# Kernel optimization log

Hardware: AMD Instinct MI355X
Metric: run time of the kernel (lower is better)

Reference implementation:

```python
import jax, jax.numpy as jnp
import numpy as np

CROP_H = 216
CROP_W = 216
NUM_CROPS = 8


def setup_inputs() -> dict:
    key = jax.random.key(0)
    k1, k2, k3 = jax.random.split(key, 3)
    B, C, H, W = 64, 3, 240, 240
    images = jax.random.normal(k1, (B, C, H, W), dtype=jnp.float32)
    crop_inds_h = jax.random.randint(k2, (B, NUM_CROPS), 0, H - CROP_H, dtype=jnp.int32)
    crop_inds_w = jax.random.randint(k3, (B, NUM_CROPS), 0, W - CROP_W, dtype=jnp.int32)
    return {"images": images, "crop_inds_h": crop_inds_h, "crop_inds_w": crop_inds_w}


def reference(images, crop_inds_h, crop_inds_w):
    # CropRandomizer.forward_in with pos_enc=True.
    B, C, H, W = images.shape
    # positional encoding channels: normalized (y, x) source-pixel coordinates
    yy, xx = jnp.meshgrid(
        jnp.arange(H, dtype=jnp.float32) / H,
        jnp.arange(W, dtype=jnp.float32) / W,
        indexing="ij",
    )
    pos = jnp.stack((yy, xx))                       # [2, H, W]
    pos = jnp.broadcast_to(pos[None], (B, 2, H, W)) # [B, 2, H, W]
    src = jnp.concatenate((images, pos), axis=1)    # [B, C+2, H, W]
    Cp = C + 2

    def crop_one(img, h0, w0):
        # img: [Cp, H, W]; h0, w0 scalar ints
        return jax.lax.dynamic_slice(img, (0, h0, w0), (Cp, CROP_H, CROP_W))

    per_image = jax.vmap(lambda img, hs, ws: jax.vmap(lambda h, w: crop_one(img, h, w))(hs, ws))
    crops = per_image(src, crop_inds_h, crop_inds_w)  # [B, N, Cp, CROP_H, CROP_W]
    return crops.reshape(B * NUM_CROPS, Cp, CROP_H, CROP_W)
```

## Files before the change

kernel.cpp:

```cpp
#include <hip/hip_runtime.h>


#define CROP_HW   216
#define N_CROPS   8
#define IMG_B     64
#define IMG_C     3
#define IMG_H     240
#define IMG_W     240
#define CP        5

#define ROW4      (CROP_HW / 4)
#define PLANE4    (CROP_HW * ROW4)
#define CROP4     (CP * PLANE4)

__global__ __launch_bounds__(256) void crop_pos_kernel(
    const float* __restrict__ images,
    const int*   __restrict__ ch,
    const int*   __restrict__ cw,
    float4*      __restrict__ out,
    unsigned int total4)
{
    const float inv = 1.0f / 240.0f;
    unsigned int stride = gridDim.x * blockDim.x;
    for (unsigned int idx = blockIdx.x * blockDim.x + threadIdx.x;
         idx < total4; idx += stride) {

        unsigned int n    = idx / CROP4;
        unsigned int rem  = idx - n * CROP4;
        unsigned int c    = rem / PLANE4;
        unsigned int rem2 = rem - c * PLANE4;
        unsigned int i    = rem2 / ROW4;
        unsigned int j    = (rem2 - i * ROW4) * 4;

        unsigned int b  = n >> 3;
        unsigned int cr = n & 7;
        int h0 = ch[b * N_CROPS + cr];
        int w0 = cw[b * N_CROPS + cr];

        float4 v;
        if (c < IMG_C) {
            const float* src = images
                + (((b * IMG_C + c) * IMG_H) + (unsigned)(h0 + (int)i)) * IMG_W
                + (unsigned)(w0 + (int)j);
            v.x = src[0]; v.y = src[1]; v.z = src[2]; v.w = src[3];
        } else if (c == 3) {
            float val = (float)(h0 + (int)i) * inv;
            v.x = val; v.y = val; v.z = val; v.w = val;
        } else {
            float base = (float)(w0 + (int)j) * inv;
            v.x = base;
            v.y = base + inv;
            v.z = base + 2.0f * inv;
            v.w = base + 3.0f * inv;
        }
        out[idx] = v;
    }
}

extern "C" void kernel_launch(void* const* d_in, const int* in_sizes, int n_in,
                              void* d_out, int out_size, void* d_ws, size_t ws_size,
                              hipStream_t stream) {
    const float* images = (const float*)d_in[0];
    const int*   ch     = (const int*)d_in[1];
    const int*   cw     = (const int*)d_in[2];
    float4*      out    = (float4*)d_out;

    unsigned int total4 = (unsigned int)(out_size / 4);
    dim3 block(256);
    dim3 grid(2048);
    crop_pos_kernel<<<grid, block, 0, stream>>>(images, ch, cw, out, total4);
}
```

Measured before the change: 533.7 us.

## Assign one block per crop plane with nontemporal vector stores

Replaces the grid-stride loop over flattened output indices with one block per (crop, channel) plane. Crop offsets and the channel branch become block-uniform, and per-element index division is reduced. Output writes use nontemporal stores so the large write stream bypasses cache retention. The fixed grid is now tied to 512 crops, so the launch no longer depends on the output size.

```diff
diff --git a/kernel.cpp b/kernel.cpp
--- a/kernel.cpp
+++ b/kernel.cpp
@@ -3,7 +3,6 @@
 
 #define CROP_HW   216
 #define N_CROPS   8
-#define IMG_B     64
 #define IMG_C     3
 #define IMG_H     240
 #define IMG_W     240
@@ -13,47 +12,58 @@
 #define PLANE4    (CROP_HW * ROW4)
 #define CROP4     (CP * PLANE4)
 
+typedef float f32x4 __attribute__((ext_vector_type(4)));
+
 __global__ __launch_bounds__(256) void crop_pos_kernel(
     const float* __restrict__ images,
     const int*   __restrict__ ch,
     const int*   __restrict__ cw,
-    float4*      __restrict__ out,
-    unsigned int total4)
+    f32x4*       __restrict__ out)
 {
     const float inv = 1.0f / 240.0f;
-    unsigned int stride = gridDim.x * blockDim.x;
-    for (unsigned int idx = blockIdx.x * blockDim.x + threadIdx.x;
-         idx < total4; idx += stride) {
 
-        unsigned int n    = idx / CROP4;
-        unsigned int rem  = idx - n * CROP4;
-        unsigned int c    = rem / PLANE4;
-        unsigned int rem2 = rem - c * PLANE4;
-        unsigned int i    = rem2 / ROW4;
-        unsigned int j    = (rem2 - i * ROW4) * 4;
+    unsigned int blk = blockIdx.x;
+    unsigned int n   = blk / CP;
+    unsigned int c   = blk - n * CP;
+    unsigned int b   = n >> 3;
+    unsigned int cr  = n & 7;
 
-        unsigned int b  = n >> 3;
-        unsigned int cr = n & 7;
-        int h0 = ch[b * N_CROPS + cr];
-        int w0 = cw[b * N_CROPS + cr];
+    int h0 = ch[b * N_CROPS + cr];
+    int w0 = cw[b * N_CROPS + cr];
 
-        float4 v;
-        if (c < IMG_C) {
-            const float* src = images
-                + (((b * IMG_C + c) * IMG_H) + (unsigned)(h0 + (int)i)) * IMG_W
-                + (unsigned)(w0 + (int)j);
-            v.x = src[0]; v.y = src[1]; v.z = src[2]; v.w = src[3];
-        } else if (c == 3) {
+    f32x4* outp = out + (size_t)n * CROP4 + (size_t)c * PLANE4;
+
+    if (c < IMG_C) {
+        const float* src0 = images
+            + (((size_t)(b * IMG_C + c) * IMG_H) + (unsigned)h0) * IMG_W
+            + (unsigned)w0;
+        for (unsigned int t = threadIdx.x; t < PLANE4; t += 256) {
+            unsigned int i  = t / ROW4;
+            unsigned int j  = (t - i * ROW4) * 4;
+            const float* s  = src0 + i * IMG_W + j;
+            f32x4 v;
+            v.x = s[0]; v.y = s[1]; v.z = s[2]; v.w = s[3];
+            __builtin_nontemporal_store(v, &outp[t]);
+        }
+    } else if (c == 3) {
+        for (unsigned int t = threadIdx.x; t < PLANE4; t += 256) {
+            unsigned int i = t / ROW4;
             float val = (float)(h0 + (int)i) * inv;
-            v.x = val; v.y = val; v.z = val; v.w = val;
-        } else {
+            f32x4 v; v.x = val; v.y = val; v.z = val; v.w = val;
+            __builtin_nontemporal_store(v, &outp[t]);
+        }
+    } else {
+        for (unsigned int t = threadIdx.x; t < PLANE4; t += 256) {
+            unsigned int i = t / ROW4;
+            unsigned int j = (t - i * ROW4) * 4;
             float base = (float)(w0 + (int)j) * inv;
+            f32x4 v;
             v.x = base;
             v.y = base + inv;
             v.z = base + 2.0f * inv;
             v.w = base + 3.0f * inv;
+            __builtin_nontemporal_store(v, &outp[t]);
         }
-        out[idx] = v;
     }
 }
 
@@ -63,10 +73,9 @@
     const float* images = (const float*)d_in[0];
     const int*   ch     = (const int*)d_in[1];
     const int*   cw     = (const int*)d_in[2];
-    float4*      out    = (float4*)d_out;
+    f32x4*       out    = (f32x4*)d_out;
 
-    unsigned int total4 = (unsigned int)(out_size / 4);
     dim3 block(256);
-    dim3 grid(2048);
-    crop_pos_kernel<<<grid, block, 0, stream>>>(images, ch, cw, out, total4);
+    dim3 grid(512 * CP);
+    crop_pos_kernel<<<grid, block, 0, stream>>>(images, ch, cw, out);
 }
```

New measurement: 543.4 us. Within noise of the previous version (+1.8%).
